# Kernel tuning notes

Hardware: AMD Instinct MI355X
Metric: run time of the kernel (lower is better)

Reference implementation:

```python
import jax, jax.numpy as jnp
import numpy as np

B, C, H, W = 4, 8, 384, 384
NUM_LAYERS = 5
CG_ITERS = 10


def conv2d(x, w, b):
    # x: [B,Cin,H,W], w: [Cout,Cin,3,3]
    y = jax.lax.conv_general_dilated(x, w, (1, 1), 'SAME',
                                     dimension_numbers=('NCHW', 'OIHW', 'NCHW'))
    return y + b[None, :, None, None]


def dw(x, w_in, b_in, ws_mid, bs_mid, w_out, b_out):
    # Sequence: conv, conv, relu, conv, conv, relu, conv, conv, relu, conv, conv, relu, conv
    h = conv2d(x, w_in, b_in)
    for i in range(7):
        h = conv2d(h, ws_mid[i], bs_mid[i])
        if i % 2 == 0:  # ReLU after convs 2,4,6,8
            h = jax.nn.relu(h)
    h = conv2d(h, w_out, b_out)
    return x + h  # residual


def conjugate_grad(rhs, csm_c, mask, lam):
    # rhs: [B,H,W] complex; csm_c: [B,C,H,W] complex; mask: [B,H,W] real
    def AtA(p):
        coil = csm_c * p[:, None]                      # [B,C,H,W]
        k = jnp.fft.fft2(coil) * mask[:, None]         # masked k-space
        return jnp.sum(jnp.conj(csm_c) * jnp.fft.ifft2(k), axis=1)

    def body(carry, _):
        x, r, p, rTr = carry
        Ap = AtA(p) + lam * p
        pAp = jnp.sum(jnp.conj(p) * Ap, axis=(-2, -1)).real
        alpha = rTr / pAp
        x = x + alpha[:, None, None] * p
        r = r - alpha[:, None, None] * Ap
        rTrNew = jnp.sum(jnp.conj(r) * r, axis=(-2, -1)).real
        beta = rTrNew / rTr
        p = r + beta[:, None, None] * p
        return (x, r, p, rTrNew), None

    x0 = jnp.zeros_like(rhs)
    rTr0 = jnp.sum(jnp.conj(rhs) * rhs, axis=(-2, -1)).real
    (x, _, _, _), _ = jax.lax.scan(body, (x0, rhs, rhs, rTr0), None, length=CG_ITERS)
    return x


def reference(under_img, csm, mask, lam, w_in, b_in, ws_mid, bs_mid, w_out, b_out):
    csm_c = jax.lax.complex(csm[..., 0], csm[..., 1])  # [B,C,H,W] complex
    lam_s = lam[0]
    x = under_img
    for _ in range(NUM_LAYERS):
        x = dw(x, w_in, b_in, ws_mid, bs_mid, w_out, b_out)
        x = under_img + lam_s * x
        rhs = jax.lax.complex(x[:, 0], x[:, 1])        # view_as_complex(permute(0,2,3,1))
        xc = conjugate_grad(rhs, csm_c, mask, lam_s)
        x = jnp.stack([xc.real, xc.imag], axis=1)      # view_as_real -> [B,2,H,W]
    return x


def setup_inputs() -> dict:
    key = jax.random.key(0)
    ks = jax.random.split(key, 8)
    under_img = jax.random.normal(ks[0], (B, 2, H, W), jnp.float32)
    csm = jax.random.normal(ks[1], (B, C, H, W, 2), jnp.float32) / np.sqrt(C)
    mask = (jax.random.uniform(ks[2], (B, H, W)) > 0.5).astype(jnp.float32)
    lam = jnp.array([0.05], jnp.float32)
    w_in = jax.random.normal(ks[3], (64, 2, 3, 3), jnp.float32) * 0.02
    b_in = jnp.zeros((64,), jnp.float32)
    ws_mid = jax.random.normal(ks[4], (7, 64, 64, 3, 3), jnp.float32) * 0.02
    bs_mid = jnp.zeros((7, 64), jnp.float32)
    w_out = jax.random.normal(ks[5], (2, 64, 3, 3), jnp.float32) * 0.02
    b_out = jnp.zeros((2,), jnp.float32)
    return {"under_img": under_img, "csm": csm, "mask": mask, "lam": lam,
            "w_in": w_in, "b_in": b_in, "ws_mid": ws_mid, "bs_mid": bs_mid,
            "w_out": w_out, "b_out": b_out}
```

## Files before the change

### kernel.cpp

```cpp
#include <hip/hip_runtime.h>
#include <hip/hip_bf16.h>
#include <hip/hip_fp16.h>
#include <math.h>

#define HH 384
#define WW 384
#define HW (HH*WW)
#define PH 386
#define PW 386
#define BB 4
#define CC 8
#define NLAYERS 5
#define CGITERS 10
#define PI_F 3.14159265358979323846f

typedef __attribute__((ext_vector_type(8))) short short8;
typedef __attribute__((ext_vector_type(4))) float floatx4;

struct cf { float x, y; };
__device__ __forceinline__ cf cadd(cf a, cf b){ cf r; r.x=a.x+b.x; r.y=a.y+b.y; return r; }
__device__ __forceinline__ cf csub(cf a, cf b){ cf r; r.x=a.x-b.x; r.y=a.y-b.y; return r; }
__device__ __forceinline__ cf cmul(cf a, cf b){ cf r; r.x=a.x*b.x - a.y*b.y; r.y=a.x*b.y + a.y*b.x; return r; }
__device__ __forceinline__ cf csqr(cf a){ cf r; r.x = a.x*a.x - a.y*a.y; r.y = 2.f*a.x*a.y; return r; }
__device__ __forceinline__ cf shflxor(cf v, int m){ cf r; r.x = __shfl_xor(v.x, m); r.y = __shfl_xor(v.y, m); return r; }
__device__ __forceinline__ int brev7(int l){ return (int)(__brev((unsigned)l) >> 25); }
__device__ __forceinline__ int padi(int i){ return i + (i >> 3); }
__device__ __forceinline__ cf h2cf(__half2 h){ float2 f = __half22float2(h); cf r; r.x = f.x; r.y = f.y; return r; }
__device__ __forceinline__ __half2 cf2h(cf v){ return __floats2half2_rn(v.x, v.y); }

__device__ __forceinline__ void radix3(cf a0, cf a1, cf a2, float s3, cf y[3]) {
  float tx = a1.x + a2.x, ty_ = a1.y + a2.y;
  float ux = a1.x - a2.x, uy = a1.y - a2.y;
  y[0].x = a0.x + tx;              y[0].y = a0.y + ty_;
  y[1].x = a0.x - 0.5f*tx - s3*uy; y[1].y = a0.y - 0.5f*ty_ + s3*ux;
  y[2].x = a0.x - 0.5f*tx + s3*uy; y[2].y = a0.y - 0.5f*ty_ - s3*ux;
}

template<int SIGN>
__device__ __forceinline__ void fft384_wave(int l, const cf v[6], cf uA[3], cf uB[3]) {
  const float s3 = SIGN * 0.8660254037844386f;
  radix3(v[0], v[2], v[4], s3, uA);
  radix3(v[1], v[3], v[5], s3, uB);
  float sA, cA;
  __sincosf(SIGN * (2.0f * PI_F / 384.0f) * (float)l, &sA, &cA);
  cf wA1; wA1.x = cA; wA1.y = sA;
  cf wA2 = csqr(wA1);
  cf w6; w6.x = 0.5f; w6.y = s3;
  cf wB1 = cmul(wA1, w6);
  cf wB2 = csqr(wB1);
  uA[1] = cmul(uA[1], wA1); uA[2] = cmul(uA[2], wA2);
  uB[1] = cmul(uB[1], wB1); uB[2] = cmul(uB[2], wB2);
  cf u = cmul(wA2, wA1);
  #pragma unroll
  for (int k1 = 0; k1 < 3; ++k1) {
    cf a = uA[k1], b = uB[k1];
    uA[k1] = cadd(a, b);
    uB[k1] = cmul(csub(a, b), u);
  }
  #pragma unroll
  for (int h = 32; h >= 1; h >>= 1) {
    u = csqr(u);
    const bool up = (l & h) != 0;
    #pragma unroll
    for (int k1 = 0; k1 < 3; ++k1) {
      cf pa = shflxor(uA[k1], h);
      cf pb = shflxor(uB[k1], h);
      cf na = up ? cmul(csub(uA[k1], pa), u) : cadd(uA[k1], pa);
      cf nb = up ? cmul(csub(uB[k1], pb), u) : cadd(uB[k1], pb);
      uA[k1] = na; uB[k1] = nb;
    }
  }
}


__global__ void repack_mid_k(const float* __restrict__ ws_mid, __hip_bfloat16* __restrict__ wrep) {
  const int idx = blockIdx.x * 256 + threadIdx.x;
  if (idx >= 7*9*64*64) return;
  const int ci = idx & 63, co = (idx >> 6) & 63, tap = (idx >> 12) % 9, i = idx / (9*4096);
  wrep[idx] = __float2bfloat16(ws_mid[(((size_t)i*64 + co)*64 + ci)*9 + tap]);
}

__global__ void zero_border_k(__hip_bfloat16* __restrict__ a0, __hip_bfloat16* __restrict__ a1) {
  const int idx = blockIdx.x * 256 + threadIdx.x;
  if (idx >= 2*4*1540*8) return;
  const int s = idx & 7;
  int e = idx >> 3;
  const int buf = e / 6160; e -= buf*6160;
  const int b = e / 1540;  const int i = e - b*1540;
  int y, x;
  if (i < 386)       { y = 0;            x = i; }
  else if (i < 772)  { y = 385;          x = i - 386; }
  else if (i < 1156) { y = i - 772 + 1;  x = 0; }
  else               { y = i - 1156 + 1; x = 385; }
  __hip_bfloat16* p = (buf ? a1 : a0) + ((size_t)(b*PH + y)*PW + x)*64 + s*8;
  *(uint4*)p = make_uint4(0u, 0u, 0u, 0u);
}

__global__ void __launch_bounds__(256) conv_in_k(const float* __restrict__ xin,
                                                 const float* __restrict__ w,
                                                 const float* __restrict__ bias,
                                                 __hip_bfloat16* __restrict__ out) {
  __shared__ float tile[2][340];
  const int tx = threadIdx.x & 31, ty = threadIdx.x >> 5;
  const int x0 = blockIdx.x * 32, y0 = blockIdx.y * 8, b = blockIdx.z;
  for (int e = threadIdx.x; e < 680; e += 256) {
    int ci = e / 340, rr = e % 340;
    int iy = y0 - 1 + rr / 34, ix = x0 - 1 + rr % 34;
    float v = 0.f;
    if (iy >= 0 && iy < HH && ix >= 0 && ix < WW)
      v = xin[(b*2 + ci)*HW + iy*WW + ix];
    tile[ci][rr] = v;
  }
  __syncthreads();
  float acc[64];
  #pragma unroll
  for (int co = 0; co < 64; ++co) acc[co] = bias[co];
  #pragma unroll
  for (int ci = 0; ci < 2; ++ci) {
    float v0 = tile[ci][ty*34+tx],     v1 = tile[ci][ty*34+tx+1],     v2 = tile[ci][ty*34+tx+2];
    float v3 = tile[ci][(ty+1)*34+tx], v4 = tile[ci][(ty+1)*34+tx+1], v5 = tile[ci][(ty+1)*34+tx+2];
    float v6 = tile[ci][(ty+2)*34+tx], v7 = tile[ci][(ty+2)*34+tx+1], v8 = tile[ci][(ty+2)*34+tx+2];
    #pragma unroll
    for (int co = 0; co < 64; ++co) {
      const float* wp = w + co*18 + ci*9;
      float a = acc[co];
      a = fmaf(v0, wp[0], a); a = fmaf(v1, wp[1], a); a = fmaf(v2, wp[2], a);
      a = fmaf(v3, wp[3], a); a = fmaf(v4, wp[4], a); a = fmaf(v5, wp[5], a);
      a = fmaf(v6, wp[6], a); a = fmaf(v7, wp[7], a); a = fmaf(v8, wp[8], a);
      acc[co] = a;
    }
  }
  const size_t obase = ((size_t)(b*PH + y0 + ty + 1)*PW + (x0 + tx + 1))*64;
  #pragma unroll
  for (int s = 0; s < 8; ++s) {
    uint4 u;
    __hip_bfloat16* hp = (__hip_bfloat16*)&u;
    #pragma unroll
    for (int j = 0; j < 8; ++j) hp[j] = __float2bfloat16(acc[s*8 + j]);
    *(uint4*)(out + obase + s*8) = u;
  }
}

__global__ void __launch_bounds__(256) conv_mid_mfma_k(
    const __hip_bfloat16* __restrict__ in,
    const __hip_bfloat16* __restrict__ wrep,
    const float* __restrict__ bias,
    __hip_bfloat16* __restrict__ out, int relu) {
  __shared__ __hip_bfloat16 otile[256*72];
  const int tid = threadIdx.x;
  const int l = tid & 63, wv = tid >> 6;
  const int x0 = blockIdx.x * 32, y0 = blockIdx.y * 8, b = blockIdx.z;

  const int kseg = l >> 4;
  const int lr = l & 15;

  floatx4 acc[4][4];
  #pragma unroll
  for (int mt = 0; mt < 4; ++mt)
    #pragma unroll
    for (int nt = 0; nt < 4; ++nt)
      acc[mt][nt] = (floatx4){0.f, 0.f, 0.f, 0.f};

  const __hip_bfloat16* wlane = wrep + lr*64 + kseg*8;
  short8 bf[4][2];
  #pragma unroll
  for (int nt = 0; nt < 4; ++nt) {
    bf[nt][0] = *(const short8*)(wlane + nt*1024);
    bf[nt][1] = *(const short8*)(wlane + nt*1024 + 32);
  }

  const __hip_bfloat16* inb = in + ((size_t)(b*PH + y0 + 2*wv)*PW + x0)*64 + kseg*8;

  #pragma unroll 1
  for (int tap = 0; tap < 9; ++tap) {
    short8 bfn[4][2];
    if (tap < 8) {
      const __hip_bfloat16* wn = wlane + (tap + 1)*4096;
      #pragma unroll
      for (int nt = 0; nt < 4; ++nt) {
        bfn[nt][0] = *(const short8*)(wn + nt*1024);
        bfn[nt][1] = *(const short8*)(wn + nt*1024 + 32);
      }
    }
    const int dy = tap / 3, dx = tap - dy*3;
    short8 af[4][2];
    #pragma unroll
    for (int mt = 0; mt < 4; ++mt) {
      const __hip_bfloat16* ap = inb + (((mt >> 1) + dy)*PW + (mt & 1)*16 + lr + dx)*64;
      af[mt][0] = *(const short8*)(ap);
      af[mt][1] = *(const short8*)(ap + 32);
    }
    #pragma unroll
    for (int mt = 0; mt < 4; ++mt)
      #pragma unroll
      for (int nt = 0; nt < 4; ++nt) {
        acc[mt][nt] = __builtin_amdgcn_mfma_f32_16x16x32_bf16(af[mt][0], bf[nt][0], acc[mt][nt], 0, 0, 0);
        acc[mt][nt] = __builtin_amdgcn_mfma_f32_16x16x32_bf16(af[mt][1], bf[nt][1], acc[mt][nt], 0, 0, 0);
      }
    if (tap < 8) {
      #pragma unroll
      for (int nt = 0; nt < 4; ++nt) { bf[nt][0] = bfn[nt][0]; bf[nt][1] = bfn[nt][1]; }
    }
  }

  #pragma unroll
  for (int mt = 0; mt < 4; ++mt) {
    const int row = 2*wv + (mt >> 1);
    #pragma unroll
    for (int nt = 0; nt < 4; ++nt) {
      const int ch = nt*16 + lr;
      const float bv = bias[ch];
      #pragma unroll
      for (int rr = 0; rr < 4; ++rr) {
        const int px = (mt & 1)*16 + kseg*4 + rr;
        float v = acc[mt][nt][rr] + bv;
        if (relu) v = fmaxf(v, 0.f);
        otile[(row*32 + px)*72 + ch] = __float2bfloat16(v);
      }
    }
  }
  __syncthreads();
  #pragma unroll
  for (int iter = 0; iter < 8; ++iter) {
    const int p = iter*32 + (tid >> 3), s = tid & 7;
    const int row = p >> 5, px = p & 31;
    uint4 v = *(const uint4*)(&otile[p*72 + s*8]);
    *(uint4*)(out + ((size_t)(b*PH + y0 + row + 1)*PW + (x0 + px + 1))*64 + s*8) = v;
  }
}

__global__ void __launch_bounds__(256) conv_out_k(const __hip_bfloat16* __restrict__ in,
                                                  const float* __restrict__ w,
                                                  const float* __restrict__ bias,
                                                  const float* __restrict__ xcur,
                                                  const float* __restrict__ under,
                                                  const float* __restrict__ lam,
                                                  cf* __restrict__ r, cf* __restrict__ p,
                                                  cf* __restrict__ xc, float* __restrict__ scL) {
  __shared__ __hip_bfloat16 atile[340*72];
  __shared__ float wl[2*64*9];
  __shared__ float wsum[4];
  const int tid = threadIdx.x;
  const int tx = tid & 31, ty = tid >> 5;
  const int x0 = blockIdx.x * 32, y0 = blockIdx.y * 8, b = blockIdx.z;

  for (int e = tid; e < 340*8; e += 256) {
    int pp = e >> 3, s = e & 7;
    uint4 v = *(const uint4*)(in + ((size_t)(b*PH + y0 + pp/34)*PW + (x0 + pp%34))*64 + s*8);
    *(uint4*)(&atile[pp*72 + s*8]) = v;
  }
  for (int e = tid; e < 2*64*9; e += 256) wl[e] = w[e];
  __syncthreads();

  float a0 = bias[0], a1 = bias[1];
  #pragma unroll 1
  for (int tap = 0; tap < 9; ++tap) {
    const int dy = tap / 3, dx = tap - dy*3;
    const __hip_bfloat16* ap = &atile[((ty + dy)*34 + tx + dx)*72];
    #pragma unroll
    for (int s = 0; s < 8; ++s) {
      short8 v8 = *(const short8*)(ap + s*8);
      const __hip_bfloat16* hv = (const __hip_bfloat16*)&v8;
      #pragma unroll
      for (int j = 0; j < 8; ++j) {
        const float f = __bfloat162float(hv[j]);
        a0 = fmaf(f, wl[(s*8 + j)*9 + tap], a0);
        a1 = fmaf(f, wl[(64 + s*8 + j)*9 + tap], a1);
      }
    }
  }
  const float lamv = lam[0];
  const int y = y0 + ty, x = x0 + tx;
  const int idx2 = y*WW + x;
  float xv0 = xcur[b*2*HW + idx2],  xv1 = xcur[b*2*HW + HW + idx2];
  float u0  = under[b*2*HW + idx2], u1  = under[b*2*HW + HW + idx2];
  float r0 = u0 + lamv * (xv0 + a0);
  float r1 = u1 + lamv * (xv1 + a1);
  const int cidx = b*HW + idx2;
  cf vv; vv.x = r0; vv.y = r1;
  r[cidx] = vv; p[cidx] = vv;
  cf zz; zz.x = 0.f; zz.y = 0.f; xc[cidx] = zz;
  float partial = r0*r0 + r1*r1;
  for (int off = 32; off; off >>= 1) partial += __shfl_down(partial, off);
  const int l = tid & 63, wvid = tid >> 6;
  if (l == 0) wsum[wvid] = partial;
  __syncthreads();
  if (tid == 0) atomicAdd(&scL[b], wsum[0]+wsum[1]+wsum[2]+wsum[3]);
}


__global__ void __launch_bounds__(256) pass_a_k(const cf* __restrict__ rold, cf* __restrict__ rnew,
                                                const cf* __restrict__ pold, cf* __restrict__ pnew,
                                                cf* __restrict__ xc, const cf* __restrict__ Ap,
                                                const cf* __restrict__ csm, __half2* __restrict__ t,
                                                float* __restrict__ scL, int it) {
  __shared__ cf rowbuf[4][434];
  const int l = threadIdx.x & 63, wv = threadIdx.x >> 6;
  const int y = blockIdx.x * 4 + wv;
  const int c = blockIdx.y, b = blockIdx.z;
  const int rowoff = b*HW + y*WW;
  cf pv[6];
  if (it == 0) {
    #pragma unroll
    for (int m = 0; m < 6; ++m) pv[m] = pold[rowoff + l + 64*m];
  } else {
    const float rtrp  = scL[(it-1)*4 + b];
    const float pApp  = scL[40 + (it-1)*4 + b];
    const float ApApp = scL[80 + (it-1)*4 + b];
    const float alpha = rtrp / pApp;
    const float rtrn  = alpha*alpha*ApApp - rtrp;
    const float beta  = rtrn / rtrp;
    if (blockIdx.x == 0 && c == 0 && threadIdx.x == 0) scL[it*4 + b] = rtrn;
    #pragma unroll
    for (int m = 0; m < 6; ++m) {
      const int idx = rowoff + l + 64*m;
      cf rv = rold[idx];
      cf av = Ap[idx];
      rv.x -= alpha*av.x; rv.y -= alpha*av.y;
      cf po = pold[idx];
      pv[m].x = rv.x + beta*po.x; pv[m].y = rv.y + beta*po.y;
      if (c == 0) {
        rnew[idx] = rv;
        pnew[idx] = pv[m];
        cf xv = xc[idx]; xv.x += alpha*po.x; xv.y += alpha*po.y; xc[idx] = xv;
      }
    }
  }
  const cf* crow = csm + (b*CC + c)*HW + y*WW;
  cf v[6];
  #pragma unroll
  for (int m = 0; m < 6; ++m) v[m] = cmul(crow[l + 64*m], pv[m]);
  cf uA[3], uB[3];
  fft384_wave<-1>(l, v, uA, uB);
  const int R3 = 3 * brev7(l);
  cf* rb = rowbuf[wv];
  #pragma unroll
  for (int k1 = 0; k1 < 3; ++k1) { rb[padi(k1 + R3)] = uA[k1]; rb[padi(k1 + R3 + 3)] = uB[k1]; }
  __half2* trow = t + (b*CC + c)*HW + y*WW;
  #pragma unroll
  for (int m = 0; m < 6; ++m) trow[l + 64*m] = cf2h(rb[padi(l + 64*m)]);
}

__global__ void __launch_bounds__(256) pass_b_k(__half2* __restrict__ t, const float* __restrict__ mask) {
  __shared__ cf tile[431*9];
  const int b = blockIdx.z, c = blockIdx.y, x0 = blockIdx.x * 8;
  __half2* base = t + (b*CC + c)*HW;
  for (int e = threadIdx.x; e < 3072; e += 256) {
    int y = e >> 3, xx = e & 7;
    tile[padi(y)*9 + xx] = h2cf(base[y*WW + x0 + xx]);
  }
  __syncthreads();
  const int l = threadIdx.x & 63, wv = threadIdx.x >> 6;
  const int R3 = 3 * brev7(l);
  for (int rep = 0; rep < 2; ++rep) {
    const int xx = wv*2 + rep, x = x0 + xx;
    cf v[6];
    #pragma unroll
    for (int m = 0; m < 6; ++m) v[m] = tile[padi(l + 64*m)*9 + xx];
    cf uA[3], uB[3];
    fft384_wave<-1>(l, v, uA, uB);
    const float* mrow = mask + b*HW + x;
    #pragma unroll
    for (int k1 = 0; k1 < 3; ++k1) {
      float mA = mrow[(k1 + R3)*WW], mB = mrow[(k1 + R3 + 3)*WW];
      uA[k1].x *= mA; uA[k1].y *= mA; uB[k1].x *= mB; uB[k1].y *= mB;
    }
    __syncthreads();
    #pragma unroll
    for (int k1 = 0; k1 < 3; ++k1) { tile[padi(k1 + R3)*9 + xx] = uA[k1]; tile[padi(k1 + R3 + 3)*9 + xx] = uB[k1]; }
    __syncthreads();
    #pragma unroll
    for (int m = 0; m < 6; ++m) v[m] = tile[padi(l + 64*m)*9 + xx];
    fft384_wave<1>(l, v, uA, uB);
    const float s = 1.0f / 384.0f;
    #pragma unroll
    for (int k1 = 0; k1 < 3; ++k1) {
      uA[k1].x *= s; uA[k1].y *= s; uB[k1].x *= s; uB[k1].y *= s;
      tile[padi(k1 + R3)*9 + xx] = uA[k1]; tile[padi(k1 + R3 + 3)*9 + xx] = uB[k1];
    }
    __syncthreads();
  }
  for (int e = threadIdx.x; e < 3072; e += 256) {
    int y = e >> 3, xx = e & 7;
    base[y*WW + x0 + xx] = cf2h(tile[padi(y)*9 + xx]);
  }
}

__global__ void __launch_bounds__(256) pass_c_k(const __half2* __restrict__ t, const cf* __restrict__ csm,
                                                const cf* __restrict__ p, cf* __restrict__ Ap,
                                                const float* __restrict__ lam,
                                                float* __restrict__ scL, int it) {
  __shared__ cf rowbuf[4][434];
  __shared__ cf redbuf[3][384];
  const int l = threadIdx.x & 63, wv = threadIdx.x >> 6;
  const int y = blockIdx.x, b = blockIdx.y;
  const int R3 = 3 * brev7(l);
  cf* rb = rowbuf[wv];
  cf acc[6] = {};
  #pragma unroll 1
  for (int ci = 0; ci < 2; ++ci) {
    const int c = wv*2 + ci;
    const __half2* trow = t + (b*CC + c)*HW + y*WW;
    cf v[6];
    #pragma unroll
    for (int m = 0; m < 6; ++m) v[m] = h2cf(trow[l + 64*m]);
    cf uA[3], uB[3];
    fft384_wave<1>(l, v, uA, uB);
    #pragma unroll
    for (int k1 = 0; k1 < 3; ++k1) { rb[padi(k1 + R3)] = uA[k1]; rb[padi(k1 + R3 + 3)] = uB[k1]; }
    const cf* crow = csm + (b*CC + c)*HW + y*WW;
    #pragma unroll
    for (int m = 0; m < 6; ++m) {
      cf cs = crow[l + 64*m];
      cf wz = rb[padi(l + 64*m)];
      acc[m].x += cs.x*wz.x + cs.y*wz.y;
      acc[m].y += cs.x*wz.y - cs.y*wz.x;
    }
  }
  if (wv > 0) {
    #pragma unroll
    for (int m = 0; m < 6; ++m) redbuf[wv - 1][l + 64*m] = acc[m];
  }
  __syncthreads();
  if (wv == 0) {
    #pragma unroll
    for (int m = 0; m < 6; ++m) {
      #pragma unroll
      for (int j = 0; j < 3; ++j) {
        cf o = redbuf[j][l + 64*m];
        acc[m].x += o.x; acc[m].y += o.y;
      }
    }
    const float lamv = lam[0];
    const float sc384 = 1.0f / 384.0f;
    const cf* prow = p + b*HW + y*WW;
    cf* aprow = Ap + b*HW + y*WW;
    float partial = 0.f, partial2 = 0.f;
    #pragma unroll
    for (int m = 0; m < 6; ++m) {
      cf pv = prow[l + 64*m];
      cf ap; ap.x = acc[m].x*sc384 + lamv*pv.x; ap.y = acc[m].y*sc384 + lamv*pv.y;
      aprow[l + 64*m] = ap;
      partial  += pv.x*ap.x + pv.y*ap.y;
      partial2 += ap.x*ap.x + ap.y*ap.y;
    }
    #pragma unroll
    for (int off = 32; off; off >>= 1) {
      partial  += __shfl_down(partial, off);
      partial2 += __shfl_down(partial2, off);
    }
    if (l == 0) {
      atomicAdd(&scL[40 + it*4 + b], partial);
      atomicAdd(&scL[80 + it*4 + b], partial2);
    }
  }
}

__global__ void __launch_bounds__(256) final_x_k(const cf* __restrict__ xc, const cf* __restrict__ p9,
                                                 const float* __restrict__ scL, float* __restrict__ out) {
  const int idx = blockIdx.x * 256 + threadIdx.x;
  const int b = idx / HW;
  const int rem = idx - b*HW;
  const float alpha = scL[(CGITERS-1)*4 + b] / scL[40 + (CGITERS-1)*4 + b];
  cf xv = xc[idx], pv = p9[idx];
  xv.x += alpha*pv.x; xv.y += alpha*pv.y;
  out[b*2*HW + rem] = xv.x;
  out[b*2*HW + HW + rem] = xv.y;
}

__global__ void zero_sc_k(float* sc) {
  for (int i = threadIdx.x; i < NLAYERS*128; i += 256) sc[i] = 0.f;
}

extern "C" void kernel_launch(void* const* d_in, const int* in_sizes, int n_in,
                              void* d_out, int out_size, void* d_ws, size_t ws_size,
                              hipStream_t stream) {
  (void)in_sizes; (void)n_in; (void)out_size; (void)ws_size;
  const float* under  = (const float*)d_in[0];
  const cf*    csm    = (const cf*)d_in[1];
  const float* mask   = (const float*)d_in[2];
  const float* lam    = (const float*)d_in[3];
  const float* w_in   = (const float*)d_in[4];
  const float* b_in   = (const float*)d_in[5];
  const float* ws_mid = (const float*)d_in[6];
  const float* bs_mid = (const float*)d_in[7];
  const float* w_out  = (const float*)d_in[8];
  const float* b_out  = (const float*)d_in[9];
  float* xcur = (float*)d_out;

  char* bws = (char*)d_ws;
  size_t off = 0;
  auto carve = [&](size_t bytes) { char* pp = bws + off; off += (bytes + 255) & ~(size_t)255; return (void*)pp; };
  __hip_bfloat16* actA = (__hip_bfloat16*)carve((size_t)BB*PH*PW*64*2);
  __hip_bfloat16* actB = (__hip_bfloat16*)carve((size_t)BB*PH*PW*64*2);
  __half2* t = (__half2*)carve((size_t)BB*CC*HW*4);
  cf* rbuf0 = (cf*)carve((size_t)BB*HW*8);
  cf* rbuf1 = (cf*)carve((size_t)BB*HW*8);
  cf* pbuf0 = (cf*)carve((size_t)BB*HW*8);
  cf* pbuf1 = (cf*)carve((size_t)BB*HW*8);
  cf* xc    = (cf*)carve((size_t)BB*HW*8);
  cf* Ap    = (cf*)carve((size_t)BB*HW*8);
  float* sc = (float*)carve(4096);
  __hip_bfloat16* wrep = (__hip_bfloat16*)carve((size_t)7*9*64*64*2);

  hipMemcpyAsync(xcur, under, (size_t)BB*2*HW*sizeof(float), hipMemcpyDeviceToDevice, stream);

  zero_sc_k<<<1, 256, 0, stream>>>(sc);
  zero_border_k<<<(2*4*1540*8 + 255)/256, 256, 0, stream>>>(actA, actB);
  repack_mid_k<<<(7*9*64*64 + 255)/256, 256, 0, stream>>>(ws_mid, wrep);

  dim3 cgrid(WW/32, HH/8, BB);
  dim3 agrid(HH/4, CC, BB);
  dim3 bgrid(WW/8, CC, BB);
  dim3 c2grid(HH, BB);
  const int egrid = BB*HW/256;

  __hip_bfloat16* bufs[2] = { actA, actB };
  cf* rb[2] = { rbuf0, rbuf1 };
  cf* pb[2] = { pbuf0, pbuf1 };

  for (int layer = 0; layer < NLAYERS; ++layer) {
    float* scL = sc + layer*128;
    conv_in_k<<<cgrid, 256, 0, stream>>>(xcur, w_in, b_in, bufs[0]);
    for (int i = 0; i < 7; ++i) {
      conv_mid_mfma_k<<<cgrid, 256, 0, stream>>>(bufs[i & 1], wrep + (size_t)i*9*4096,
                                                 bs_mid + i*64, bufs[(i + 1) & 1], (i % 2 == 0) ? 1 : 0);
    }
    conv_out_k<<<cgrid, 256, 0, stream>>>(bufs[1], w_out, b_out, xcur, under, lam,
                                          rbuf0, pbuf0, xc, scL);
    for (int it = 0; it < CGITERS; ++it) {
      cf* rold = rb[(it + 1) & 1];
      cf* rnew = rb[it & 1];
      cf* pold = pb[(it + 1) & 1];
      cf* pnew = pb[it & 1];
      if (it == 0) { rold = rbuf0; pold = pbuf0; rnew = rbuf0; pnew = pbuf0; }
      pass_a_k<<<agrid, 256, 0, stream>>>(rold, rnew, pold, pnew, xc, Ap, csm, t, scL, it);
      pass_b_k<<<bgrid, 256, 0, stream>>>(t, mask);
      pass_c_k<<<c2grid, 256, 0, stream>>>(t, csm, pnew, Ap, lam, scL, it);
    }
    final_x_k<<<egrid, 256, 0, stream>>>(xc, pb[(CGITERS - 1) & 1], scL, xcur);
  }
}
```

Before: 10.87 ms.

## Stage conv input tile in LDS and restructure CG updates into pass_c

The mid conv kernel now loads a 10x34 halo tile of bf16 activations into shared memory once and reads the MFMA A-fragments from LDS instead of global memory for each of the nine taps. The CG iteration moves the x and r updates into pass_c, so pass_a only forms p. pAp is computed by Parseval: lam*||p||^2 from pass_a plus the masked k-space energy from pass_b. This drops the Ap buffer and the final_x kernel and removes several full-array reads and writes per iteration. The cost is extra reductions and atomics, plus an fp16-based pAp estimate that may shift numerics.

```diff
diff --git a/kernel.cpp b/kernel.cpp
--- a/kernel.cpp
+++ b/kernel.cpp
@@ -146,20 +146,26 @@
     const __hip_bfloat16* __restrict__ wrep,
     const float* __restrict__ bias,
     __hip_bfloat16* __restrict__ out, int relu) {
-  __shared__ __hip_bfloat16 otile[256*72];
+  __shared__ __hip_bfloat16 atile[10*34*72];
   const int tid = threadIdx.x;
   const int l = tid & 63, wv = tid >> 6;
   const int x0 = blockIdx.x * 32, y0 = blockIdx.y * 8, b = blockIdx.z;
 
+  for (int e = tid; e < 340*8; e += 256) {
+    int p = e >> 3, s = e & 7;
+    uint4 v = *(const uint4*)(in + ((size_t)(b*PH + y0 + p/34)*PW + (x0 + p%34))*64 + s*8);
+    *(uint4*)(&atile[p*72 + s*8]) = v;
+  }
+
+  floatx4 acc[4][4];
+  #pragma unroll
+  for (int mt = 0; mt < 4; ++mt)
+    #pragma unroll
+    for (int nt = 0; nt < 4; ++nt)
+      acc[mt][nt] = (floatx4){0.f, 0.f, 0.f, 0.f};
+
   const int kseg = l >> 4;
   const int lr = l & 15;
-
-  floatx4 acc[4][4];
-  #pragma unroll
-  for (int mt = 0; mt < 4; ++mt)
-    #pragma unroll
-    for (int nt = 0; nt < 4; ++nt)
-      acc[mt][nt] = (floatx4){0.f, 0.f, 0.f, 0.f};
 
   const __hip_bfloat16* wlane = wrep + lr*64 + kseg*8;
   short8 bf[4][2];
@@ -169,7 +175,7 @@
     bf[nt][1] = *(const short8*)(wlane + nt*1024 + 32);
   }
 
-  const __hip_bfloat16* inb = in + ((size_t)(b*PH + y0 + 2*wv)*PW + x0)*64 + kseg*8;
+  __syncthreads();
 
   #pragma unroll 1
   for (int tap = 0; tap < 9; ++tap) {
@@ -186,7 +192,9 @@
     short8 af[4][2];
     #pragma unroll
     for (int mt = 0; mt < 4; ++mt) {
-      const __hip_bfloat16* ap = inb + (((mt >> 1) + dy)*PW + (mt & 1)*16 + lr + dx)*64;
+      const int ry = 2*wv + (mt >> 1) + dy;
+      const int px = (mt & 1)*16 + lr + dx;
+      const __hip_bfloat16* ap = &atile[(ry*34 + px)*72 + kseg*8];
       af[mt][0] = *(const short8*)(ap);
       af[mt][1] = *(const short8*)(ap + 32);
     }
@@ -203,6 +211,8 @@
     }
   }
 
+  __syncthreads();
+  __hip_bfloat16* otile = atile;
   #pragma unroll
   for (int mt = 0; mt < 4; ++mt) {
     const int row = 2*wv + (mt >> 1);
@@ -289,41 +299,34 @@
 }
 
 
-__global__ void __launch_bounds__(256) pass_a_k(const cf* __restrict__ rold, cf* __restrict__ rnew,
+__global__ void __launch_bounds__(256) pass_a_k(const cf* __restrict__ rres,
                                                 const cf* __restrict__ pold, cf* __restrict__ pnew,
-                                                cf* __restrict__ xc, const cf* __restrict__ Ap,
                                                 const cf* __restrict__ csm, __half2* __restrict__ t,
+                                                const float* __restrict__ lam,
                                                 float* __restrict__ scL, int it) {
   __shared__ cf rowbuf[4][434];
+  __shared__ float wsum[4];
   const int l = threadIdx.x & 63, wv = threadIdx.x >> 6;
   const int y = blockIdx.x * 4 + wv;
   const int c = blockIdx.y, b = blockIdx.z;
   const int rowoff = b*HW + y*WW;
   cf pv[6];
+  float pnorm = 0.f;
   if (it == 0) {
     #pragma unroll
-    for (int m = 0; m < 6; ++m) pv[m] = pold[rowoff + l + 64*m];
+    for (int m = 0; m < 6; ++m) {
+      pv[m] = pold[rowoff + l + 64*m];
+      pnorm += pv[m].x*pv[m].x + pv[m].y*pv[m].y;
+    }
   } else {
-    const float rtrp  = scL[(it-1)*4 + b];
-    const float pApp  = scL[40 + (it-1)*4 + b];
-    const float ApApp = scL[80 + (it-1)*4 + b];
-    const float alpha = rtrp / pApp;
-    const float rtrn  = alpha*alpha*ApApp - rtrp;
-    const float beta  = rtrn / rtrp;
-    if (blockIdx.x == 0 && c == 0 && threadIdx.x == 0) scL[it*4 + b] = rtrn;
+    const float beta = scL[it*4 + b] / scL[(it-1)*4 + b];
     #pragma unroll
     for (int m = 0; m < 6; ++m) {
       const int idx = rowoff + l + 64*m;
-      cf rv = rold[idx];
-      cf av = Ap[idx];
-      rv.x -= alpha*av.x; rv.y -= alpha*av.y;
-      cf po = pold[idx];
+      cf rv = rres[idx], po = pold[idx];
       pv[m].x = rv.x + beta*po.x; pv[m].y = rv.y + beta*po.y;
-      if (c == 0) {
-        rnew[idx] = rv;
-        pnew[idx] = pv[m];
-        cf xv = xc[idx]; xv.x += alpha*po.x; xv.y += alpha*po.y; xc[idx] = xv;
-      }
+      pnorm += pv[m].x*pv[m].x + pv[m].y*pv[m].y;
+      if (c == 0) pnew[idx] = pv[m];
     }
   }
   const cf* crow = csm + (b*CC + c)*HW + y*WW;
@@ -339,10 +342,20 @@
   __half2* trow = t + (b*CC + c)*HW + y*WW;
   #pragma unroll
   for (int m = 0; m < 6; ++m) trow[l + 64*m] = cf2h(rb[padi(l + 64*m)]);
-}
-
-__global__ void __launch_bounds__(256) pass_b_k(__half2* __restrict__ t, const float* __restrict__ mask) {
+  if (c == 0) {
+    #pragma unroll
+    for (int off = 32; off; off >>= 1) pnorm += __shfl_down(pnorm, off);
+    if (l == 0) wsum[wv] = pnorm;
+    __syncthreads();
+    if (threadIdx.x == 0)
+      atomicAdd(&scL[48 + it*4 + b], lam[0] * (wsum[0]+wsum[1]+wsum[2]+wsum[3]));
+  }
+}
+
+__global__ void __launch_bounds__(256) pass_b_k(__half2* __restrict__ t, const float* __restrict__ mask,
+                                                float* __restrict__ scL, int it) {
   __shared__ cf tile[431*9];
+  __shared__ float wsumB[4];
   const int b = blockIdx.z, c = blockIdx.y, x0 = blockIdx.x * 8;
   __half2* base = t + (b*CC + c)*HW;
   for (int e = threadIdx.x; e < 3072; e += 256) {
@@ -352,6 +365,7 @@
   __syncthreads();
   const int l = threadIdx.x & 63, wv = threadIdx.x >> 6;
   const int R3 = 3 * brev7(l);
+  float kss = 0.f;
   for (int rep = 0; rep < 2; ++rep) {
     const int xx = wv*2 + rep, x = x0 + xx;
     cf v[6];
@@ -364,6 +378,7 @@
     for (int k1 = 0; k1 < 3; ++k1) {
       float mA = mrow[(k1 + R3)*WW], mB = mrow[(k1 + R3 + 3)*WW];
       uA[k1].x *= mA; uA[k1].y *= mA; uB[k1].x *= mB; uB[k1].y *= mB;
+      kss += uA[k1].x*uA[k1].x + uA[k1].y*uA[k1].y + uB[k1].x*uB[k1].x + uB[k1].y*uB[k1].y;
     }
     __syncthreads();
     #pragma unroll
@@ -384,12 +399,19 @@
     int y = e >> 3, xx = e & 7;
     base[y*WW + x0 + xx] = cf2h(tile[padi(y)*9 + xx]);
   }
+  #pragma unroll
+  for (int off = 32; off; off >>= 1) kss += __shfl_down(kss, off);
+  if (l == 0) wsumB[wv] = kss;
+  __syncthreads();
+  if (threadIdx.x == 0)
+    atomicAdd(&scL[48 + it*4 + b], (wsumB[0]+wsumB[1]+wsumB[2]+wsumB[3]) * (1.0f/147456.0f));
 }
 
 __global__ void __launch_bounds__(256) pass_c_k(const __half2* __restrict__ t, const cf* __restrict__ csm,
-                                                const cf* __restrict__ p, cf* __restrict__ Ap,
-                                                const float* __restrict__ lam,
-                                                float* __restrict__ scL, int it) {
+                                                const cf* __restrict__ p, cf* __restrict__ rres,
+                                                cf* __restrict__ xc, const float* __restrict__ lam,
+                                                float* __restrict__ scL, int it,
+                                                float* __restrict__ xout) {
   __shared__ cf rowbuf[4][434];
   __shared__ cf redbuf[3][384];
   const int l = threadIdx.x & 63, wv = threadIdx.x >> 6;
@@ -433,39 +455,30 @@
     }
     const float lamv = lam[0];
     const float sc384 = 1.0f / 384.0f;
-    const cf* prow = p + b*HW + y*WW;
-    cf* aprow = Ap + b*HW + y*WW;
-    float partial = 0.f, partial2 = 0.f;
+    const float alpha = scL[it*4 + b] / scL[48 + it*4 + b];
+    const int rowoff = b*HW + y*WW;
+    float partial = 0.f;
     #pragma unroll
     for (int m = 0; m < 6; ++m) {
-      cf pv = prow[l + 64*m];
+      const int idx = rowoff + l + 64*m;
+      cf pv = p[idx];
       cf ap; ap.x = acc[m].x*sc384 + lamv*pv.x; ap.y = acc[m].y*sc384 + lamv*pv.y;
-      aprow[l + 64*m] = ap;
-      partial  += pv.x*ap.x + pv.y*ap.y;
-      partial2 += ap.x*ap.x + ap.y*ap.y;
-    }
-    #pragma unroll
-    for (int off = 32; off; off >>= 1) {
-      partial  += __shfl_down(partial, off);
-      partial2 += __shfl_down(partial2, off);
-    }
-    if (l == 0) {
-      atomicAdd(&scL[40 + it*4 + b], partial);
-      atomicAdd(&scL[80 + it*4 + b], partial2);
-    }
-  }
-}
-
-__global__ void __launch_bounds__(256) final_x_k(const cf* __restrict__ xc, const cf* __restrict__ p9,
-                                                 const float* __restrict__ scL, float* __restrict__ out) {
-  const int idx = blockIdx.x * 256 + threadIdx.x;
-  const int b = idx / HW;
-  const int rem = idx - b*HW;
-  const float alpha = scL[(CGITERS-1)*4 + b] / scL[40 + (CGITERS-1)*4 + b];
-  cf xv = xc[idx], pv = p9[idx];
-  xv.x += alpha*pv.x; xv.y += alpha*pv.y;
-  out[b*2*HW + rem] = xv.x;
-  out[b*2*HW + HW + rem] = xv.y;
+      cf xv = xc[idx]; xv.x += alpha*pv.x; xv.y += alpha*pv.y;
+      cf rv = rres[idx]; rv.x -= alpha*ap.x; rv.y -= alpha*ap.y;
+      rres[idx] = rv;
+      partial += rv.x*rv.x + rv.y*rv.y;
+      if (it == CGITERS - 1) {
+        const int rem = y*WW + l + 64*m;
+        xout[b*2*HW + rem] = xv.x;
+        xout[b*2*HW + HW + rem] = xv.y;
+      } else {
+        xc[idx] = xv;
+      }
+    }
+    #pragma unroll
+    for (int off = 32; off; off >>= 1) partial += __shfl_down(partial, off);
+    if (l == 0) atomicAdd(&scL[(it+1)*4 + b], partial);
+  }
 }
 
 __global__ void zero_sc_k(float* sc) {
@@ -495,11 +508,9 @@
   __hip_bfloat16* actB = (__hip_bfloat16*)carve((size_t)BB*PH*PW*64*2);
   __half2* t = (__half2*)carve((size_t)BB*CC*HW*4);
   cf* rbuf0 = (cf*)carve((size_t)BB*HW*8);
-  cf* rbuf1 = (cf*)carve((size_t)BB*HW*8);
   cf* pbuf0 = (cf*)carve((size_t)BB*HW*8);
   cf* pbuf1 = (cf*)carve((size_t)BB*HW*8);
   cf* xc    = (cf*)carve((size_t)BB*HW*8);
-  cf* Ap    = (cf*)carve((size_t)BB*HW*8);
   float* sc = (float*)carve(4096);
   __hip_bfloat16* wrep = (__hip_bfloat16*)carve((size_t)7*9*64*64*2);
 
@@ -513,10 +524,8 @@
   dim3 agrid(HH/4, CC, BB);
   dim3 bgrid(WW/8, CC, BB);
   dim3 c2grid(HH, BB);
-  const int egrid = BB*HW/256;
 
   __hip_bfloat16* bufs[2] = { actA, actB };
-  cf* rb[2] = { rbuf0, rbuf1 };
   cf* pb[2] = { pbuf0, pbuf1 };
 
   for (int layer = 0; layer < NLAYERS; ++layer) {
@@ -529,15 +538,11 @@
     conv_out_k<<<cgrid, 256, 0, stream>>>(bufs[1], w_out, b_out, xcur, under, lam,
                                           rbuf0, pbuf0, xc, scL);
     for (int it = 0; it < CGITERS; ++it) {
-      cf* rold = rb[(it + 1) & 1];
-      cf* rnew = rb[it & 1];
-      cf* pold = pb[(it + 1) & 1];
-      cf* pnew = pb[it & 1];
-      if (it == 0) { rold = rbuf0; pold = pbuf0; rnew = rbuf0; pnew = pbuf0; }
-      pass_a_k<<<agrid, 256, 0, stream>>>(rold, rnew, pold, pnew, xc, Ap, csm, t, scL, it);
-      pass_b_k<<<bgrid, 256, 0, stream>>>(t, mask);
-      pass_c_k<<<c2grid, 256, 0, stream>>>(t, csm, pnew, Ap, lam, scL, it);
-    }
-    final_x_k<<<egrid, 256, 0, stream>>>(xc, pb[(CGITERS - 1) & 1], scL, xcur);
-  }
-}
+      cf* pold = (it == 0) ? pbuf0 : pb[(it + 1) & 1];
+      cf* pnew = (it == 0) ? pbuf0 : pb[it & 1];
+      pass_a_k<<<agrid, 256, 0, stream>>>(rbuf0, pold, pnew, csm, t, lam, scL, it);
+      pass_b_k<<<bgrid, 256, 0, stream>>>(t, mask, scL, it);
+      pass_c_k<<<c2grid, 256, 0, stream>>>(t, csm, pnew, rbuf0, xc, lam, scL, it, xcur);
+    }
+  }
+}
```

Measured after the change: 10.06 ms. -7.4%, faster.
